# Performance work log

Measured on AMD Instinct MI355X. Metric: run time of the kernel, lower is better.

Reference implementation:

```python
import jax, jax.numpy as jnp
import numpy as np

BLANK_ID = 0


def bias_norm(x, bias, log_scale):
    # icefall BiasNorm: x * exp(log_scale) / rms(x - bias), rms over channel dim
    scales = jnp.exp(log_scale) * jax.lax.rsqrt(
        jnp.mean(jnp.square(x - bias), axis=-1, keepdims=True))
    return x * scales


def setup_inputs() -> dict:
    key = jax.random.key(0)
    N, T, S = 16, 400, 5
    ENC, DEC, JOINT, V = 512, 512, 512, 2000
    OV = V - 1  # out_vocab_dim
    ks = jax.random.split(key, 16)
    f = jax.random.normal
    return {
        "encoder_out": f(ks[0], (N, T, S, ENC), jnp.float32),
        "blank_decoder_out": f(ks[1], (N, T, S, DEC), jnp.float32),
        "vocab_decoder_out": f(ks[2], (N, T, S, DEC), jnp.float32),
        # fc_encoder_proj + its BiasNorm
        "W_enc": f(ks[3], (JOINT, ENC), jnp.float32) * 0.02,
        "b_enc": jnp.zeros((JOINT,), jnp.float32),
        "bn_enc_bias": f(ks[4], (JOINT,), jnp.float32) * 0.01,
        "bn_enc_log_scale": jnp.zeros((), jnp.float32),
        # fc_blank_decoder + its BiasNorm
        "W_bdec": f(ks[5], (JOINT, DEC), jnp.float32) * 0.02,
        "b_bdec": jnp.zeros((JOINT,), jnp.float32),
        "bn_bdec_bias": f(ks[6], (JOINT,), jnp.float32) * 0.01,
        "bn_bdec_log_scale": jnp.zeros((), jnp.float32),
        # BiasNorm for vocab decoder path (over decoder_hidden_dim)
        "bn_vdec_bias": f(ks[7], (DEC,), jnp.float32) * 0.01,
        "bn_vdec_log_scale": jnp.zeros((), jnp.float32),
        # output heads
        "W_blank": f(ks[8], (1, JOINT), jnp.float32) * 0.02,
        "b_blank": jnp.zeros((1,), jnp.float32),
        "W_ev": f(ks[9], (OV, JOINT), jnp.float32) * 0.02,
        "b_ev": jnp.zeros((OV,), jnp.float32),
        "W_dv": f(ks[10], (OV, JOINT), jnp.float32) * 0.02,
        "b_dv": jnp.zeros((OV,), jnp.float32),
    }


def reference(encoder_out, blank_decoder_out, vocab_decoder_out,
              W_enc, b_enc, bn_enc_bias, bn_enc_log_scale,
              W_bdec, b_bdec, bn_bdec_bias, bn_bdec_log_scale,
              bn_vdec_bias, bn_vdec_log_scale,
              W_blank, b_blank, W_ev, b_ev, W_dv, b_dv):
    # encoder_proj: ScaledLinear -> BiasNorm
    enc = bias_norm(jnp.einsum('ntsc,jc->ntsj', encoder_out, W_enc) + b_enc,
                    bn_enc_bias, bn_enc_log_scale)
    # blank_decoder_proj: ScaledLinear -> BiasNorm
    bdec = bias_norm(jnp.einsum('ntsc,jc->ntsj', blank_decoder_out, W_bdec) + b_bdec,
                     bn_bdec_bias, bn_bdec_log_scale)
    # vocab_decoder_proj: BiasNorm -> ScaledLinear -> log_softmax
    vdec = bias_norm(vocab_decoder_out, bn_vdec_bias, bn_vdec_log_scale)
    vdec = jnp.einsum('ntsj,vj->ntsv', vdec, W_dv) + b_dv
    vocab_decoder_prob = jax.nn.log_softmax(vdec, axis=-1)
    # joint
    blank_prob = jnp.einsum('ntsj,oj->ntso', jax.nn.relu(enc + bdec), W_blank) + b_blank
    vocab_prob = jnp.einsum('ntsj,vj->ntsv', enc, W_ev) + b_ev + vocab_decoder_prob
    out = jnp.concatenate(
        [vocab_prob[..., :BLANK_ID], blank_prob, vocab_prob[..., BLANK_ID:]], axis=-1)
    return out, vocab_decoder_prob
```

## Files before the change

kernel.cpp:

```cpp
#include <hip/hip_runtime.h>


#define R_TOTAL 32000
#define OV 1999
#define WG_ROWS 2049

typedef __attribute__((ext_vector_type(8))) short bh8;
typedef __attribute__((ext_vector_type(4))) float fx4;

__device__ __forceinline__ unsigned short f2bf(float f) {
  union { float f; unsigned u; } v; v.f = f;
  unsigned r = v.u + 0x7fffu + ((v.u >> 16) & 1u);
  return (unsigned short)(r >> 16);
}
__device__ __forceinline__ float bf2f(unsigned short h) {
  union { unsigned u; float f; } v; v.u = ((unsigned)h) << 16;
  return v.f;
}
__device__ __forceinline__ void gload_lds16(const void* g, void* l) {
  __builtin_amdgcn_global_load_lds(
      (__attribute__((address_space(1))) void*)g,
      (__attribute__((address_space(3))) void*)l, 16, 0, 0);
}
__device__ __forceinline__ void st16u(float* dst, const float* src) {
  float v[4] = {src[0], src[1], src[2], src[3]};
  __builtin_memcpy((void*)dst, v, 16);
}

__global__ void wconv_kernel(const float* __restrict__ src, unsigned short* __restrict__ dst,
                             int src_rows, int dst_rows, int shift) {
  long long n = (long long)dst_rows * 512;
  for (long long i = (long long)blockIdx.x * blockDim.x + threadIdx.x; i < n;
       i += (long long)gridDim.x * blockDim.x) {
    int row = (int)(i >> 9);
    int sr = row - shift;
    dst[i] = (sr >= 0 && sr < src_rows) ? f2bf(src[(long long)sr * 512 + (i & 511)])
                                        : (unsigned short)0;
  }
}

template<int MODE>
__global__ __launch_bounds__(1024)
void proj_norm_kernel(const float* __restrict__ X,
                      const unsigned short* __restrict__ Wb,
                      const float* __restrict__ b_lin,
                      const float* __restrict__ bn_bias,
                      const float* __restrict__ log_scale,
                      unsigned short* __restrict__ enc_b,
                      const float* __restrict__ W_blank,
                      const float* __restrict__ b_blank,
                      float* __restrict__ blank)
{
  __shared__ __attribute__((aligned(16))) unsigned short As[128 * 64];
  __shared__ __attribute__((aligned(16))) unsigned short Bs[512 * 64];
  __shared__ float red[8][128];
  __shared__ float scale_s[128];

  const int tid = threadIdx.x;
  const int l  = tid & 63;
  const int lq = l >> 4;
  const int lr = l & 15;
  const int w  = tid >> 6;
  const int wr = w >> 3;
  const int wc = w & 7;
  const int rowBase = blockIdx.x * 128;

  char* AsB = (char*)As;
  char* BsB = (char*)Bs;

  fx4 acc[4][4];
#pragma unroll
  for (int m = 0; m < 4; ++m)
#pragma unroll
    for (int n = 0; n < 4; ++n)
#pragma unroll
      for (int r = 0; r < 4; ++r) acc[m][n][r] = 0.f;

  for (int kt = 0; kt < 8; ++kt) {
#pragma unroll
    for (int p = 0; p < 2; ++p) {
      int g = tid + p * 1024;
      int row = g >> 4;
      int c4  = g & 15;
      const float4 v = *(const float4*)(X + (long long)(rowBase + row) * 512 + kt * 64 + c4 * 4);
      ushort4 h;
      h.x = f2bf(v.x); h.y = f2bf(v.y); h.z = f2bf(v.z); h.w = f2bf(v.w);
      *(ushort4*)(AsB + row * 128 + ((c4 * 8) ^ ((row & 7) << 4))) = h;
    }
#pragma unroll
    for (int p = 0; p < 4; ++p) {
      int gb = (w * 4 + p) * 64;
      int g = gb + l;
      int row = g >> 3;
      int c8 = (g & 7) ^ (row & 7);
      gload_lds16(Wb + (long long)row * 512 + kt * 64 + c8 * 8, BsB + gb * 16);
    }
    __syncthreads();

#pragma unroll
    for (int kk = 0; kk < 2; ++kk) {
      const int kb = (kk * 32 + lq * 8) * 2;
      bh8 a[4];
#pragma unroll
      for (int m = 0; m < 4; ++m) {
        int row = wr * 64 + m * 16 + lr;
        a[m] = *(const bh8*)(AsB + row * 128 + (kb ^ ((row & 7) << 4)));
      }
#pragma unroll
      for (int n = 0; n < 4; ++n) {
        int brow = wc * 64 + n * 16 + lr;
        bh8 bfr = *(const bh8*)(BsB + brow * 128 + (kb ^ ((brow & 7) << 4)));
#pragma unroll
        for (int m = 0; m < 4; ++m)
          acc[m][n] = __builtin_amdgcn_mfma_f32_16x16x32_bf16(a[m], bfr, acc[m][n], 0, 0, 0);
      }
    }
    __syncthreads();
  }

  const float escale = expf(log_scale[0]);
  float bl[4], bb[4], wb[4];
#pragma unroll
  for (int n = 0; n < 4; ++n) {
    int col = wc * 64 + n * 16 + lr;
    bl[n] = b_lin[col];
    bb[n] = bn_bias[col];
    if (MODE == 1) wb[n] = W_blank[col];
  }

  float ps[4][4];
#pragma unroll
  for (int m = 0; m < 4; ++m)
#pragma unroll
    for (int r = 0; r < 4; ++r) ps[m][r] = 0.f;
#pragma unroll
  for (int m = 0; m < 4; ++m)
#pragma unroll
    for (int n = 0; n < 4; ++n)
#pragma unroll
      for (int r = 0; r < 4; ++r) {
        float v = acc[m][n][r] + bl[n];
        float d = v - bb[n];
        ps[m][r] += d * d;
      }
#pragma unroll
  for (int off = 1; off < 16; off <<= 1)
#pragma unroll
    for (int m = 0; m < 4; ++m)
#pragma unroll
      for (int r = 0; r < 4; ++r)
        ps[m][r] += __shfl_xor(ps[m][r], off);

  if (lr == 0) {
#pragma unroll
    for (int m = 0; m < 4; ++m)
#pragma unroll
      for (int r = 0; r < 4; ++r)
        red[wc][wr * 64 + m * 16 + lq * 4 + r] = ps[m][r];
  }
  __syncthreads();
  if (tid < 128) {
    float s = 0.f;
#pragma unroll
    for (int c = 0; c < 8; ++c) s += red[c][tid];
    scale_s[tid] = escale * rsqrtf(s * (1.0f / 512.0f));
  }
  __syncthreads();

  if (MODE == 0) {
#pragma unroll
    for (int m = 0; m < 4; ++m)
#pragma unroll
      for (int n = 0; n < 4; ++n)
#pragma unroll
        for (int r = 0; r < 4; ++r) {
          int rl = wr * 64 + m * 16 + lq * 4 + r;
          int col = wc * 64 + n * 16 + lr;
          float v = (acc[m][n][r] + bl[n]) * scale_s[rl];
          enc_b[(long long)(rowBase + rl) * 512 + col] = f2bf(v);
        }
  } else {
    float pb[4][4];
#pragma unroll
    for (int m = 0; m < 4; ++m)
#pragma unroll
      for (int r = 0; r < 4; ++r) pb[m][r] = 0.f;
#pragma unroll
    for (int m = 0; m < 4; ++m)
#pragma unroll
      for (int n = 0; n < 4; ++n)
#pragma unroll
        for (int r = 0; r < 4; ++r) {
          int rl = wr * 64 + m * 16 + lq * 4 + r;
          int col = wc * 64 + n * 16 + lr;
          float v = (acc[m][n][r] + bl[n]) * scale_s[rl];
          float e = bf2f(enc_b[(long long)(rowBase + rl) * 512 + col]);
          float s = e + v;
          s = s > 0.f ? s : 0.f;
          pb[m][r] += s * wb[n];
        }
#pragma unroll
    for (int off = 1; off < 16; off <<= 1)
#pragma unroll
      for (int m = 0; m < 4; ++m)
#pragma unroll
        for (int r = 0; r < 4; ++r)
          pb[m][r] += __shfl_xor(pb[m][r], off);
    if (lr == 0) {
#pragma unroll
      for (int m = 0; m < 4; ++m)
#pragma unroll
        for (int r = 0; r < 4; ++r)
          red[wc][wr * 64 + m * 16 + lq * 4 + r] = pb[m][r];
    }
    __syncthreads();
    if (tid < 128) {
      float s = 0.f;
#pragma unroll
      for (int c = 0; c < 8; ++c) s += red[c][tid];
      blank[rowBase + tid] = s + b_blank[0];
    }
  }
}

__global__ __launch_bounds__(256)
void vdec_norm_kernel(const float* __restrict__ X, const float* __restrict__ bn_bias,
                      const float* __restrict__ log_scale, unsigned short* __restrict__ dst)
{
  const int l = threadIdx.x & 63;
  const long long row = (long long)blockIdx.x * 4 + (threadIdx.x >> 6);
  const float* xr = X + row * 512 + l * 8;
  float4 v0 = *(const float4*)xr;
  float4 v1 = *(const float4*)(xr + 4);
  float xv[8] = {v0.x, v0.y, v0.z, v0.w, v1.x, v1.y, v1.z, v1.w};
  const float4 b0 = *(const float4*)(bn_bias + l * 8);
  const float4 b1 = *(const float4*)(bn_bias + l * 8 + 4);
  float bv[8] = {b0.x, b0.y, b0.z, b0.w, b1.x, b1.y, b1.z, b1.w};
  float s = 0.f;
#pragma unroll
  for (int i = 0; i < 8; ++i) { float d = xv[i] - bv[i]; s += d * d; }
#pragma unroll
  for (int off = 1; off < 64; off <<= 1) s += __shfl_xor(s, off);
  const float sc = expf(log_scale[0]) * rsqrtf(s * (1.0f / 512.0f));
  bh8 o;
#pragma unroll
  for (int i = 0; i < 8; ++i) o[i] = (short)f2bf(xv[i] * sc);
  *(bh8*)(dst + row * 512 + l * 8) = o;
}

__device__ __forceinline__ void xcd_swz_250x16(int& bx, int& by) {
  int bid = blockIdx.y * 250 + blockIdx.x;
  int g = (bid & 7) * 500 + (bid >> 3);
  bx = g >> 4;
  by = g & 15;
}

__global__ __launch_bounds__(256, 2)
void gemm_stats_kernel(const unsigned short* __restrict__ Abf,
                       const unsigned short* __restrict__ Wb,
                       const float* __restrict__ bias,
                       float2* __restrict__ stats)
{
  __shared__ __attribute__((aligned(16))) unsigned short As[128 * 64];
  __shared__ __attribute__((aligned(16))) unsigned short Bs[128 * 64];
  __shared__ float smax[2][128];
  __shared__ float ssum[2][128];
  const int tid = threadIdx.x;
  const int l  = tid & 63, lq = l >> 4, lr = l & 15;
  const int w  = tid >> 6;
  const int wr = w >> 1, wc = w & 1;
  int bx, by;
  xcd_swz_250x16(bx, by);
  const int rowBase = bx * 128;
  const int colBase = by * 128;
  char* AsB = (char*)As;
  char* BsB = (char*)Bs;

  fx4 acc[4][4];
#pragma unroll
  for (int m = 0; m < 4; ++m)
#pragma unroll
    for (int n = 0; n < 4; ++n)
#pragma unroll
      for (int r = 0; r < 4; ++r) acc[m][n][r] = 0.f;

  for (int kt = 0; kt < 8; ++kt) {
#pragma unroll
    for (int p = 0; p < 4; ++p) {
      int gb = (w * 4 + p) * 64;
      int g = gb + l;
      int row = g >> 3;
      int c8 = (g & 7) ^ (row & 7);
      gload_lds16(Abf + (long long)(rowBase + row) * 512 + kt * 64 + c8 * 8, AsB + gb * 16);
      gload_lds16(Wb  + (long long)(colBase + row) * 512 + kt * 64 + c8 * 8, BsB + gb * 16);
    }
    __syncthreads();
#pragma unroll
    for (int kk = 0; kk < 2; ++kk) {
      const int kb = (kk * 32 + lq * 8) * 2;
      bh8 a[4];
#pragma unroll
      for (int m = 0; m < 4; ++m) {
        int row = wr * 64 + m * 16 + lr;
        a[m] = *(const bh8*)(AsB + row * 128 + (kb ^ ((row & 7) << 4)));
      }
#pragma unroll
      for (int n = 0; n < 4; ++n) {
        int brow = wc * 64 + n * 16 + lr;
        bh8 bfr = *(const bh8*)(BsB + brow * 128 + (kb ^ ((brow & 7) << 4)));
#pragma unroll
        for (int m = 0; m < 4; ++m)
          acc[m][n] = __builtin_amdgcn_mfma_f32_16x16x32_bf16(a[m], bfr, acc[m][n], 0, 0, 0);
      }
    }
    __syncthreads();
  }

  float bl[4]; bool cv[4];
#pragma unroll
  for (int n = 0; n < 4; ++n) {
    int col = colBase + wc * 64 + n * 16 + lr;
    cv[n] = (col < OV);
    bl[n] = cv[n] ? bias[col] : 0.f;
  }

  float mloc[4][4];
#pragma unroll
  for (int m = 0; m < 4; ++m)
#pragma unroll
    for (int r = 0; r < 4; ++r) mloc[m][r] = -3.4e38f;
#pragma unroll
  for (int m = 0; m < 4; ++m)
#pragma unroll
    for (int n = 0; n < 4; ++n)
      if (cv[n])
#pragma unroll
        for (int r = 0; r < 4; ++r)
          mloc[m][r] = fmaxf(mloc[m][r], acc[m][n][r] + bl[n]);
#pragma unroll
  for (int off = 1; off < 16; off <<= 1)
#pragma unroll
    for (int m = 0; m < 4; ++m)
#pragma unroll
      for (int r = 0; r < 4; ++r)
        mloc[m][r] = fmaxf(mloc[m][r], __shfl_xor(mloc[m][r], off));
  if (lr == 0) {
#pragma unroll
    for (int m = 0; m < 4; ++m)
#pragma unroll
      for (int r = 0; r < 4; ++r)
        smax[wc][wr * 64 + m * 16 + lq * 4 + r] = mloc[m][r];
  }
  __syncthreads();
  float M[4][4];
#pragma unroll
  for (int m = 0; m < 4; ++m)
#pragma unroll
    for (int r = 0; r < 4; ++r) {
      int row = wr * 64 + m * 16 + lq * 4 + r;
      M[m][r] = fmaxf(smax[0][row], smax[1][row]);
    }
  float sl[4][4];
#pragma unroll
  for (int m = 0; m < 4; ++m)
#pragma unroll
    for (int r = 0; r < 4; ++r) sl[m][r] = 0.f;
#pragma unroll
  for (int m = 0; m < 4; ++m)
#pragma unroll
    for (int n = 0; n < 4; ++n)
      if (cv[n]) {
#pragma unroll
        for (int r = 0; r < 4; ++r) {
          float v = acc[m][n][r] + bl[n];
          sl[m][r] += __expf(v - M[m][r]);
        }
      }
#pragma unroll
  for (int off = 1; off < 16; off <<= 1)
#pragma unroll
    for (int m = 0; m < 4; ++m)
#pragma unroll
      for (int r = 0; r < 4; ++r)
        sl[m][r] += __shfl_xor(sl[m][r], off);
  if (lr == 0) {
#pragma unroll
    for (int m = 0; m < 4; ++m)
#pragma unroll
      for (int r = 0; r < 4; ++r)
        ssum[wc][wr * 64 + m * 16 + lq * 4 + r] = sl[m][r];
  }
  __syncthreads();
  if (tid < 128) {
    float2 st;
    st.x = fmaxf(smax[0][tid], smax[1][tid]);
    st.y = ssum[0][tid] + ssum[1][tid];
    stats[(long long)by * R_TOTAL + rowBase + tid] = st;
  }
}

__global__ __launch_bounds__(256)
void lz_kernel(const float2* __restrict__ stats, float* __restrict__ lz)
{
  int row = blockIdx.x * 256 + threadIdx.x;
  if (row >= R_TOTAL) return;
  float2 st[16];
  float M = -3.4e38f;
#pragma unroll
  for (int i = 0; i < 16; ++i) {
    st[i] = stats[(long long)i * R_TOTAL + row];
    M = fmaxf(M, st[i].x);
  }
  float S = 0.f;
#pragma unroll
  for (int i = 0; i < 16; ++i) S += st[i].y * __expf(st[i].x - M);
  lz[row] = M + logf(S);
}

__global__ __launch_bounds__(256, 2)
void gemm_fused_kernel(const unsigned short* __restrict__ Av_g,
                       const unsigned short* __restrict__ Ae_g,
                       const unsigned short* __restrict__ Wdv_g,
                       const unsigned short* __restrict__ Wev_g,
                       const float* __restrict__ b_dv,
                       const float* __restrict__ b_ev,
                       const float* __restrict__ lz,
                       const float* __restrict__ blank,
                       float* __restrict__ vdp,
                       float* __restrict__ outp)
{
  __shared__ __attribute__((aligned(16))) unsigned short As[128 * 64];
  __shared__ __attribute__((aligned(16))) unsigned short Bs[128 * 64];
  const int tid = threadIdx.x;
  const int l  = tid & 63, lq = l >> 4, lr = l & 15;
  const int w  = tid >> 6;
  const int wr = w >> 1, wc = w & 1;
  int bx, by;
  xcd_swz_250x16(bx, by);
  const int rowBase = bx * 128;
  const int colBase = by * 128;
  char* AsB = (char*)As;
  char* BsB = (char*)Bs;

  fx4 accV[4][4], accE[4][4];
#pragma unroll
  for (int m = 0; m < 4; ++m)
#pragma unroll
    for (int n = 0; n < 4; ++n)
#pragma unroll
      for (int r = 0; r < 4; ++r) { accV[m][n][r] = 0.f; accE[m][n][r] = 0.f; }

  for (int kt = 0; kt < 8; ++kt) {
#pragma unroll
    for (int p = 0; p < 4; ++p) {
      int gb = (w * 4 + p) * 64;
      int g = gb + l;
      int row = g >> 3;
      int c8 = (g & 7) ^ (row & 7);
      gload_lds16(Av_g  + (long long)(rowBase + row) * 512 + kt * 64 + c8 * 8, AsB + gb * 16);
      gload_lds16(Wdv_g + (long long)(colBase + row) * 512 + kt * 64 + c8 * 8, BsB + gb * 16);
    }
    __syncthreads();
#pragma unroll
    for (int kk = 0; kk < 2; ++kk) {
      const int kb = (kk * 32 + lq * 8) * 2;
      bh8 a[4];
#pragma unroll
      for (int m = 0; m < 4; ++m) {
        int row = wr * 64 + m * 16 + lr;
        a[m] = *(const bh8*)(AsB + row * 128 + (kb ^ ((row & 7) << 4)));
      }
#pragma unroll
      for (int n = 0; n < 4; ++n) {
        int brow = wc * 64 + n * 16 + lr;
        bh8 bfr = *(const bh8*)(BsB + brow * 128 + (kb ^ ((brow & 7) << 4)));
#pragma unroll
        for (int m = 0; m < 4; ++m)
          accV[m][n] = __builtin_amdgcn_mfma_f32_16x16x32_bf16(a[m], bfr, accV[m][n], 0, 0, 0);
      }
    }
    __syncthreads();
  }

  for (int kt = 0; kt < 8; ++kt) {
#pragma unroll
    for (int p = 0; p < 4; ++p) {
      int gb = (w * 4 + p) * 64;
      int g = gb + l;
      int row = g >> 3;
      int c8 = (g & 7) ^ (row & 7);
      gload_lds16(Ae_g  + (long long)(rowBase + row) * 512 + kt * 64 + c8 * 8, AsB + gb * 16);
      gload_lds16(Wev_g + (long long)(colBase + row) * 512 + kt * 64 + c8 * 8, BsB + gb * 16);
    }
    __syncthreads();
#pragma unroll
    for (int kk = 0; kk < 2; ++kk) {
      const int kb = (kk * 32 + lq * 8) * 2;
      bh8 a[4];
#pragma unroll
      for (int m = 0; m < 4; ++m) {
        int row = wr * 64 + m * 16 + lr;
        a[m] = *(const bh8*)(AsB + row * 128 + (kb ^ ((row & 7) << 4)));
      }
#pragma unroll
      for (int n = 0; n < 4; ++n) {
        int brow = wc * 64 + n * 16 + lr;
        bh8 bfr = *(const bh8*)(BsB + brow * 128 + (kb ^ ((brow & 7) << 4)));
#pragma unroll
        for (int m = 0; m < 4; ++m)
          accE[m][n] = __builtin_amdgcn_mfma_f32_16x16x32_bf16(a[m], bfr, accE[m][n], 0, 0, 0);
      }
    }
    __syncthreads();
  }

  float lzv[4][4];
#pragma unroll
  for (int m = 0; m < 4; ++m)
#pragma unroll
    for (int r = 0; r < 4; ++r)
      lzv[m][r] = lz[rowBase + wr * 64 + m * 16 + lq * 4 + r];

  float* Lvd = (float*)As;
  float* Lov = (float*)Bs;

  const int c0 = (by == 0) ? 0 : (colBase - 1);
  const int j0 = (by == 0) ? 1 : 0;
  const int Lv = min(OV, colBase + 127) - c0;

  const int flipw = (lq & 1) << 4;

#pragma unroll
  for (int c = 0; c < 4; ++c) {
    __syncthreads();
    if (wr == (c >> 1)) {
#pragma unroll
      for (int mm = 0; mm < 2; ++mm) {
        const int m = (c & 1) * 2 + mm;
#pragma unroll
        for (int n = 0; n < 4; ++n) {
          int j = wc * 64 + n * 16 + lr;
          int cg = colBase - 1 + j;
          bool v = (cg >= 0 && cg < OV);
          float bdv = v ? b_dv[cg] : 0.f;
          float bev = v ? b_ev[cg] : 0.f;
          int jx = j ^ flipw;
#pragma unroll
          for (int r = 0; r < 4; ++r) {
            int lrow = 16 * mm + lq * 4 + r;
            float vd = accV[m][n][r] + bdv - lzv[m][r];
            float ov = accE[m][n][r] + bev + vd;
            if (by == 0 && j == 0) ov = blank[rowBase + 32 * c + lrow];
            Lvd[lrow * 128 + jx] = vd;
            Lov[lrow * 128 + jx] = ov;
          }
        }
      }
    }
    __syncthreads();

#pragma unroll
    for (int pass = 0; pass < 4; ++pass) {
      int lrow = pass * 8 + (tid >> 5);
      int lane32 = tid & 31;
      int flip = ((lrow >> 2) & 1) << 4;
      long long rg = rowBase + 32 * c + lrow;
      int p = colBase + lane32 * 4;
      if (p < 2000) {
        float4 vv = *(const float4*)&Lov[lrow * 128 + ((lane32 * 4) ^ flip)];
        *(float4*)(outp + rg * 2000 + p) = vv;
      }
    }
#pragma unroll
    for (int pass = 0; pass < 4; ++pass) {
      int lrow = pass * 8 + (tid >> 5);
      int lane32 = tid & 31;
      int flip = ((lrow >> 2) & 1) << 4;
      long long rg = rowBase + 32 * c + lrow;
      int k4 = lane32 * 4;
      if (k4 < Lv) {
        float* dst = vdp + rg * OV + c0 + k4;
        int rem = Lv - k4;
        if (rem >= 4 && j0 == 0) {
          float4 vv = *(const float4*)&Lvd[lrow * 128 + (k4 ^ flip)];
          float vs[4] = {vv.x, vv.y, vv.z, vv.w};
          st16u(dst, vs);
        } else if (rem >= 4) {
          float vs[4];
#pragma unroll
          for (int q = 0; q < 4; ++q) vs[q] = Lvd[lrow * 128 + ((j0 + k4 + q) ^ flip)];
          st16u(dst, vs);
        } else {
          for (int q = 0; q < rem; ++q) dst[q] = Lvd[lrow * 128 + ((j0 + k4 + q) ^ flip)];
        }
      }
    }
  }
}

extern "C" void kernel_launch(void* const* d_in, const int* in_sizes, int n_in,
                              void* d_out, int out_size, void* d_ws, size_t ws_size,
                              hipStream_t stream) {
  const float* encoder_out  = (const float*)d_in[0];
  const float* blank_dec    = (const float*)d_in[1];
  const float* vocab_dec    = (const float*)d_in[2];
  const float* W_enc        = (const float*)d_in[3];
  const float* b_enc        = (const float*)d_in[4];
  const float* bn_enc_bias  = (const float*)d_in[5];
  const float* bn_enc_ls    = (const float*)d_in[6];
  const float* W_bdec       = (const float*)d_in[7];
  const float* b_bdec       = (const float*)d_in[8];
  const float* bn_bdec_bias = (const float*)d_in[9];
  const float* bn_bdec_ls   = (const float*)d_in[10];
  const float* bn_vdec_bias = (const float*)d_in[11];
  const float* bn_vdec_ls   = (const float*)d_in[12];
  const float* W_blank      = (const float*)d_in[13];
  const float* b_blank      = (const float*)d_in[14];
  const float* W_ev         = (const float*)d_in[15];
  const float* b_ev         = (const float*)d_in[16];
  const float* W_dv         = (const float*)d_in[17];
  const float* b_dv         = (const float*)d_in[18];

  unsigned short* Wenc_b  = (unsigned short*)d_ws;
  unsigned short* Wbdec_b = Wenc_b + 512 * 512;
  unsigned short* Wdv_g   = Wbdec_b + 512 * 512;
  unsigned short* Wev_g   = Wdv_g + (size_t)WG_ROWS * 512;
  unsigned short* enc_b   = Wev_g + (size_t)WG_ROWS * 512;
  unsigned short* vdec_b  = enc_b + (size_t)R_TOTAL * 512;
  float2* stats = (float2*)(vdec_b + (size_t)R_TOTAL * 512);
  float*  lzbuf = (float*)(stats + (size_t)R_TOTAL * 16);
  float*  blank = lzbuf + R_TOTAL;

  float* outp = (float*)d_out;
  float* vdp  = outp + (size_t)R_TOTAL * 2000;

  wconv_kernel<<<256, 256, 0, stream>>>(W_enc,  Wenc_b,  512, 512, 0);
  wconv_kernel<<<256, 256, 0, stream>>>(W_bdec, Wbdec_b, 512, 512, 0);
  wconv_kernel<<<512, 256, 0, stream>>>(W_dv,   Wdv_g,  1999, WG_ROWS, 1);
  wconv_kernel<<<512, 256, 0, stream>>>(W_ev,   Wev_g,  1999, WG_ROWS, 1);

  vdec_norm_kernel<<<8000, 256, 0, stream>>>(vocab_dec, bn_vdec_bias, bn_vdec_ls, vdec_b);
  gemm_stats_kernel<<<dim3(250, 16), 256, 0, stream>>>(vdec_b, Wdv_g + 512, b_dv, stats);
  lz_kernel<<<125, 256, 0, stream>>>(stats, lzbuf);

  proj_norm_kernel<0><<<250, 1024, 0, stream>>>(encoder_out, Wenc_b, b_enc, bn_enc_bias,
                                                bn_enc_ls, enc_b, nullptr, nullptr, nullptr);
  proj_norm_kernel<1><<<250, 1024, 0, stream>>>(blank_dec, Wbdec_b, b_bdec, bn_bdec_bias,
                                                bn_bdec_ls, enc_b, W_blank, b_blank, blank);

  gemm_fused_kernel<<<dim3(250, 16), 256, 0, stream>>>(vdec_b, enc_b, Wdv_g, Wev_g,
                                                       b_dv, b_ev, lzbuf, blank, vdp, outp);
}
```

Measured before the change: 557.7 us.

## Restructure vocab GEMMs as row-persistent blocks looping over all column tiles

```diff
diff --git a/kernel.cpp b/kernel.cpp
--- a/kernel.cpp
+++ b/kernel.cpp
@@ -248,176 +248,144 @@
   *(bh8*)(dst + row * 512 + l * 8) = o;
 }
 
-__device__ __forceinline__ void xcd_swz_250x16(int& bx, int& by) {
-  int bid = blockIdx.y * 250 + blockIdx.x;
-  int g = (bid & 7) * 500 + (bid >> 3);
-  bx = g >> 4;
-  by = g & 15;
-}
-
-__global__ __launch_bounds__(256, 2)
-void gemm_stats_kernel(const unsigned short* __restrict__ Abf,
-                       const unsigned short* __restrict__ Wb,
-                       const float* __restrict__ bias,
-                       float2* __restrict__ stats)
+__global__ __launch_bounds__(512, 2)
+void stats_kernel(const unsigned short* __restrict__ Av_g,
+                  const unsigned short* __restrict__ Wb,
+                  const float* __restrict__ bias,
+                  float* __restrict__ lzout)
 {
-  __shared__ __attribute__((aligned(16))) unsigned short As[128 * 64];
-  __shared__ __attribute__((aligned(16))) unsigned short Bs[128 * 64];
-  __shared__ float smax[2][128];
-  __shared__ float ssum[2][128];
+  __shared__ __attribute__((aligned(16))) unsigned short Wbs[2][128 * 64];
   const int tid = threadIdx.x;
   const int l  = tid & 63, lq = l >> 4, lr = l & 15;
   const int w  = tid >> 6;
-  const int wr = w >> 1, wc = w & 1;
-  int bx, by;
-  xcd_swz_250x16(bx, by);
-  const int rowBase = bx * 128;
-  const int colBase = by * 128;
-  char* AsB = (char*)As;
-  char* BsB = (char*)Bs;
-
-  fx4 acc[4][4];
-#pragma unroll
-  for (int m = 0; m < 4; ++m)
-#pragma unroll
-    for (int n = 0; n < 4; ++n)
-#pragma unroll
-      for (int r = 0; r < 4; ++r) acc[m][n][r] = 0.f;
-
-  for (int kt = 0; kt < 8; ++kt) {
-#pragma unroll
-    for (int p = 0; p < 4; ++p) {
-      int gb = (w * 4 + p) * 64;
-      int g = gb + l;
-      int row = g >> 3;
-      int c8 = (g & 7) ^ (row & 7);
-      gload_lds16(Abf + (long long)(rowBase + row) * 512 + kt * 64 + c8 * 8, AsB + gb * 16);
-      gload_lds16(Wb  + (long long)(colBase + row) * 512 + kt * 64 + c8 * 8, BsB + gb * 16);
+  const int wr = w >> 2;
+  const int wc = w & 3;
+  const int rowBase = blockIdx.x * 64;
+
+  bh8 avf[2][8][2];
+#pragma unroll
+  for (int m = 0; m < 2; ++m) {
+    const unsigned short* rp = Av_g + (long long)(rowBase + wr * 32 + m * 16 + lr) * 512;
+#pragma unroll
+    for (int kt = 0; kt < 8; ++kt)
+#pragma unroll
+      for (int kk = 0; kk < 2; ++kk)
+        avf[m][kt][kk] = *(const bh8*)(rp + kt * 64 + kk * 32 + lq * 8);
+  }
+
+  float Mx[2][4], Sx[2][4];
+#pragma unroll
+  for (int m = 0; m < 2; ++m)
+#pragma unroll
+    for (int r = 0; r < 4; ++r) { Mx[m][r] = -3.4e38f; Sx[m][r] = 0.f; }
+
+  for (int by = 0; by < 16; ++by) {
+    fx4 acc[2][2];
+#pragma unroll
+    for (int m = 0; m < 2; ++m)
+#pragma unroll
+      for (int n = 0; n < 2; ++n)
+#pragma unroll
+        for (int r = 0; r < 4; ++r) acc[m][n][r] = 0.f;
+
+#pragma unroll
+    for (int p = 0; p < 2; ++p) {
+      int lc = p * 512 + tid;
+      int rW = lc >> 3, c = lc & 7;
+      int cs = c ^ (rW & 7);
+      gload_lds16(Wb + (long long)(by * 128 + rW) * 512 + 0 * 64 + cs * 8,
+                  (char*)Wbs[0] + lc * 16);
     }
     __syncthreads();
-#pragma unroll
-    for (int kk = 0; kk < 2; ++kk) {
-      const int kb = (kk * 32 + lq * 8) * 2;
-      bh8 a[4];
-#pragma unroll
-      for (int m = 0; m < 4; ++m) {
-        int row = wr * 64 + m * 16 + lr;
-        a[m] = *(const bh8*)(AsB + row * 128 + (kb ^ ((row & 7) << 4)));
-      }
-#pragma unroll
-      for (int n = 0; n < 4; ++n) {
-        int brow = wc * 64 + n * 16 + lr;
-        bh8 bfr = *(const bh8*)(BsB + brow * 128 + (kb ^ ((brow & 7) << 4)));
-#pragma unroll
-        for (int m = 0; m < 4; ++m)
-          acc[m][n] = __builtin_amdgcn_mfma_f32_16x16x32_bf16(a[m], bfr, acc[m][n], 0, 0, 0);
-      }
-    }
-    __syncthreads();
-  }
-
-  float bl[4]; bool cv[4];
-#pragma unroll
-  for (int n = 0; n < 4; ++n) {
-    int col = colBase + wc * 64 + n * 16 + lr;
-    cv[n] = (col < OV);
-    bl[n] = cv[n] ? bias[col] : 0.f;
-  }
-
-  float mloc[4][4];
-#pragma unroll
-  for (int m = 0; m < 4; ++m)
-#pragma unroll
-    for (int r = 0; r < 4; ++r) mloc[m][r] = -3.4e38f;
-#pragma unroll
-  for (int m = 0; m < 4; ++m)
-#pragma unroll
-    for (int n = 0; n < 4; ++n)
-      if (cv[n])
-#pragma unroll
-        for (int r = 0; r < 4; ++r)
-          mloc[m][r] = fmaxf(mloc[m][r], acc[m][n][r] + bl[n]);
+
+#pragma unroll
+    for (int kt = 0; kt < 8; ++kt) {
+      if (kt < 7) {
+#pragma unroll
+        for (int p = 0; p < 2; ++p) {
+          int lc = p * 512 + tid;
+          int rW = lc >> 3, c = lc & 7;
+          int cs = c ^ (rW & 7);
+          gload_lds16(Wb + (long long)(by * 128 + rW) * 512 + (kt + 1) * 64 + cs * 8,
+                      (char*)Wbs[(kt + 1) & 1] + lc * 16);
+        }
+      }
+      char* WB = (char*)Wbs[kt & 1];
+#pragma unroll
+      for (int kk = 0; kk < 2; ++kk) {
+#pragma unroll
+        for (int n = 0; n < 2; ++n) {
+          int br = wc * 32 + n * 16 + lr;
+          bh8 bf = *(const bh8*)(WB + br * 128 + (((kk * 4 + lq) ^ (br & 7)) * 16));
+          acc[0][n] = __builtin_amdgcn_mfma_f32_16x16x32_bf16(avf[0][kt][kk], bf, acc[0][n], 0, 0, 0);
+          acc[1][n] = __builtin_amdgcn_mfma_f32_16x16x32_bf16(avf[1][kt][kk], bf, acc[1][n], 0, 0, 0);
+        }
+      }
+      __syncthreads();
+    }
+
+    int col0 = by * 128 + wc * 32 + lr;
+    int col1 = col0 + 16;
+    bool cv0 = col0 < OV, cv1 = col1 < OV;
+    float bl0 = cv0 ? bias[col0] : 0.f;
+    float bl1 = cv1 ? bias[col1] : 0.f;
+#pragma unroll
+    for (int m = 0; m < 2; ++m)
+#pragma unroll
+      for (int r = 0; r < 4; ++r) {
+        float v0 = acc[m][0][r] + bl0;
+        float v1 = acc[m][1][r] + bl1;
+        float pm = -3.4e38f;
+        if (cv0) pm = v0;
+        if (cv1) pm = fmaxf(pm, v1);
+        float s = 0.f;
+        if (cv0) s += __expf(v0 - pm);
+        if (cv1) s += __expf(v1 - pm);
+        float Mn = fmaxf(Mx[m][r], pm);
+        Sx[m][r] = Sx[m][r] * __expf(Mx[m][r] - Mn) + s * __expf(pm - Mn);
+        Mx[m][r] = Mn;
+      }
+  }
+
 #pragma unroll
   for (int off = 1; off < 16; off <<= 1)
 #pragma unroll
-    for (int m = 0; m < 4; ++m)
-#pragma unroll
-      for (int r = 0; r < 4; ++r)
-        mloc[m][r] = fmaxf(mloc[m][r], __shfl_xor(mloc[m][r], off));
+    for (int m = 0; m < 2; ++m)
+#pragma unroll
+      for (int r = 0; r < 4; ++r) {
+        float Mo = __shfl_xor(Mx[m][r], off);
+        float So = __shfl_xor(Sx[m][r], off);
+        float Mn = fmaxf(Mx[m][r], Mo);
+        Sx[m][r] = Sx[m][r] * __expf(Mx[m][r] - Mn) + So * __expf(Mo - Mn);
+        Mx[m][r] = Mn;
+      }
+
+  float2* red = (float2*)Wbs;
+  __syncthreads();
   if (lr == 0) {
 #pragma unroll
-    for (int m = 0; m < 4; ++m)
-#pragma unroll
-      for (int r = 0; r < 4; ++r)
-        smax[wc][wr * 64 + m * 16 + lq * 4 + r] = mloc[m][r];
+    for (int m = 0; m < 2; ++m)
+#pragma unroll
+      for (int r = 0; r < 4; ++r) {
+        int row = wr * 32 + m * 16 + lq * 4 + r;
+        red[wc * 64 + row] = make_float2(Mx[m][r], Sx[m][r]);
+      }
   }
   __syncthreads();
-  float M[4][4];
-#pragma unroll
-  for (int m = 0; m < 4; ++m)
-#pragma unroll
-    for (int r = 0; r < 4; ++r) {
-      int row = wr * 64 + m * 16 + lq * 4 + r;
-      M[m][r] = fmaxf(smax[0][row], smax[1][row]);
-    }
-  float sl[4][4];
-#pragma unroll
-  for (int m = 0; m < 4; ++m)
-#pragma unroll
-    for (int r = 0; r < 4; ++r) sl[m][r] = 0.f;
-#pragma unroll
-  for (int m = 0; m < 4; ++m)
-#pragma unroll
-    for (int n = 0; n < 4; ++n)
-      if (cv[n]) {
-#pragma unroll
-        for (int r = 0; r < 4; ++r) {
-          float v = acc[m][n][r] + bl[n];
-          sl[m][r] += __expf(v - M[m][r]);
-        }
-      }
-#pragma unroll
-  for (int off = 1; off < 16; off <<= 1)
-#pragma unroll
-    for (int m = 0; m < 4; ++m)
-#pragma unroll
-      for (int r = 0; r < 4; ++r)
-        sl[m][r] += __shfl_xor(sl[m][r], off);
-  if (lr == 0) {
-#pragma unroll
-    for (int m = 0; m < 4; ++m)
-#pragma unroll
-      for (int r = 0; r < 4; ++r)
-        ssum[wc][wr * 64 + m * 16 + lq * 4 + r] = sl[m][r];
-  }
-  __syncthreads();
-  if (tid < 128) {
-    float2 st;
-    st.x = fmaxf(smax[0][tid], smax[1][tid]);
-    st.y = ssum[0][tid] + ssum[1][tid];
-    stats[(long long)by * R_TOTAL + rowBase + tid] = st;
-  }
-}
-
-__global__ __launch_bounds__(256)
-void lz_kernel(const float2* __restrict__ stats, float* __restrict__ lz)
-{
-  int row = blockIdx.x * 256 + threadIdx.x;
-  if (row >= R_TOTAL) return;
-  float2 st[16];
-  float M = -3.4e38f;
-#pragma unroll
-  for (int i = 0; i < 16; ++i) {
-    st[i] = stats[(long long)i * R_TOTAL + row];
-    M = fmaxf(M, st[i].x);
-  }
-  float S = 0.f;
-#pragma unroll
-  for (int i = 0; i < 16; ++i) S += st[i].y * __expf(st[i].x - M);
-  lz[row] = M + logf(S);
-}
-
-__global__ __launch_bounds__(256, 2)
+  if (tid < 64) {
+    float M = -3.4e38f, S = 0.f;
+#pragma unroll
+    for (int c = 0; c < 4; ++c) {
+      float2 st = red[c * 64 + tid];
+      float Mn = fmaxf(M, st.x);
+      S = S * __expf(M - Mn) + st.y * __expf(st.x - Mn);
+      M = Mn;
+    }
+    lzout[rowBase + tid] = M + logf(S);
+  }
+}
+
+__global__ __launch_bounds__(512, 2)
 void gemm_fused_kernel(const unsigned short* __restrict__ Av_g,
                        const unsigned short* __restrict__ Ae_g,
                        const unsigned short* __restrict__ Wdv_g,
@@ -429,171 +397,192 @@
                        float* __restrict__ vdp,
                        float* __restrict__ outp)
 {
-  __shared__ __attribute__((aligned(16))) unsigned short As[128 * 64];
-  __shared__ __attribute__((aligned(16))) unsigned short Bs[128 * 64];
+  __shared__ __attribute__((aligned(16))) unsigned short Aes[64 * 512];
+  __shared__ __attribute__((aligned(16))) unsigned short Wbs[2][128 * 64];
   const int tid = threadIdx.x;
   const int l  = tid & 63, lq = l >> 4, lr = l & 15;
   const int w  = tid >> 6;
-  const int wr = w >> 1, wc = w & 1;
-  int bx, by;
-  xcd_swz_250x16(bx, by);
-  const int rowBase = bx * 128;
-  const int colBase = by * 128;
-  char* AsB = (char*)As;
-  char* BsB = (char*)Bs;
-
-  fx4 accV[4][4], accE[4][4];
-#pragma unroll
-  for (int m = 0; m < 4; ++m)
-#pragma unroll
-    for (int n = 0; n < 4; ++n)
-#pragma unroll
-      for (int r = 0; r < 4; ++r) { accV[m][n][r] = 0.f; accE[m][n][r] = 0.f; }
-
-  for (int kt = 0; kt < 8; ++kt) {
-#pragma unroll
-    for (int p = 0; p < 4; ++p) {
-      int gb = (w * 4 + p) * 64;
-      int g = gb + l;
-      int row = g >> 3;
-      int c8 = (g & 7) ^ (row & 7);
-      gload_lds16(Av_g  + (long long)(rowBase + row) * 512 + kt * 64 + c8 * 8, AsB + gb * 16);
-      gload_lds16(Wdv_g + (long long)(colBase + row) * 512 + kt * 64 + c8 * 8, BsB + gb * 16);
+  const int wr = w >> 2;
+  const int wc = w & 3;
+  const int rowBase = blockIdx.x * 64;
+  char* AeB = (char*)Aes;
+
+  bh8 avf[2][8][2];
+#pragma unroll
+  for (int m = 0; m < 2; ++m) {
+    const unsigned short* rp = Av_g + (long long)(rowBase + wr * 32 + m * 16 + lr) * 512;
+#pragma unroll
+    for (int kt = 0; kt < 8; ++kt)
+#pragma unroll
+      for (int kk = 0; kk < 2; ++kk)
+        avf[m][kt][kk] = *(const bh8*)(rp + kt * 64 + kk * 32 + lq * 8);
+  }
+
+#pragma unroll
+  for (int p = 0; p < 8; ++p) {
+    int lc = p * 512 + tid;
+    int r = lc >> 6, c = lc & 63;
+    int csrc = (c & 56) | ((c & 7) ^ (r & 7));
+    gload_lds16(Ae_g + (long long)(rowBase + r) * 512 + csrc * 8, AeB + lc * 16);
+  }
+
+  float lzv[2][4];
+#pragma unroll
+  for (int m = 0; m < 2; ++m)
+#pragma unroll
+    for (int r = 0; r < 4; ++r)
+      lzv[m][r] = lz[rowBase + wr * 32 + m * 16 + lq * 4 + r];
+
+  __syncthreads();
+
+  for (int by = 0; by < 16; ++by) {
+    fx4 accV[2][2], accE[2][2];
+#pragma unroll
+    for (int m = 0; m < 2; ++m)
+#pragma unroll
+      for (int n = 0; n < 2; ++n)
+#pragma unroll
+        for (int r = 0; r < 4; ++r) { accV[m][n][r] = 0.f; accE[m][n][r] = 0.f; }
+
+#pragma unroll
+    for (int p = 0; p < 2; ++p) {
+      int lc = p * 512 + tid;
+      int rW = lc >> 3, c = lc & 7;
+      int cs = c ^ (rW & 7);
+      gload_lds16(Wdv_g + (long long)(by * 128 + rW) * 512 + cs * 8,
+                  (char*)Wbs[0] + lc * 16);
     }
     __syncthreads();
 #pragma unroll
-    for (int kk = 0; kk < 2; ++kk) {
-      const int kb = (kk * 32 + lq * 8) * 2;
-      bh8 a[4];
-#pragma unroll
-      for (int m = 0; m < 4; ++m) {
-        int row = wr * 64 + m * 16 + lr;
-        a[m] = *(const bh8*)(AsB + row * 128 + (kb ^ ((row & 7) << 4)));
-      }
-#pragma unroll
-      for (int n = 0; n < 4; ++n) {
-        int brow = wc * 64 + n * 16 + lr;
-        bh8 bfr = *(const bh8*)(BsB + brow * 128 + (kb ^ ((brow & 7) << 4)));
-#pragma unroll
-        for (int m = 0; m < 4; ++m)
-          accV[m][n] = __builtin_amdgcn_mfma_f32_16x16x32_bf16(a[m], bfr, accV[m][n], 0, 0, 0);
-      }
+    for (int kt = 0; kt < 8; ++kt) {
+      if (kt < 7) {
+#pragma unroll
+        for (int p = 0; p < 2; ++p) {
+          int lc = p * 512 + tid;
+          int rW = lc >> 3, c = lc & 7;
+          int cs = c ^ (rW & 7);
+          gload_lds16(Wdv_g + (long long)(by * 128 + rW) * 512 + (kt + 1) * 64 + cs * 8,
+                      (char*)Wbs[(kt + 1) & 1] + lc * 16);
+        }
+      }
+      char* WB = (char*)Wbs[kt & 1];
+#pragma unroll
+      for (int kk = 0; kk < 2; ++kk) {
+#pragma unroll
+        for (int n = 0; n < 2; ++n) {
+          int br = wc * 32 + n * 16 + lr;
+          bh8 bf = *(const bh8*)(WB + br * 128 + (((kk * 4 + lq) ^ (br & 7)) * 16));
+          accV[0][n] = __builtin_amdgcn_mfma_f32_16x16x32_bf16(avf[0][kt][kk], bf, accV[0][n], 0, 0, 0);
+          accV[1][n] = __builtin_amdgcn_mfma_f32_16x16x32_bf16(avf[1][kt][kk], bf, accV[1][n], 0, 0, 0);
+        }
+      }
+      __syncthreads();
+    }
+
+#pragma unroll
+    for (int p = 0; p < 2; ++p) {
+      int lc = p * 512 + tid;
+      int rW = lc >> 3, c = lc & 7;
+      int cs = c ^ (rW & 7);
+      gload_lds16(Wev_g + (long long)(by * 128 + rW) * 512 + cs * 8,
+                  (char*)Wbs[0] + lc * 16);
     }
     __syncthreads();
-  }
-
-  for (int kt = 0; kt < 8; ++kt) {
-#pragma unroll
-    for (int p = 0; p < 4; ++p) {
-      int gb = (w * 4 + p) * 64;
-      int g = gb + l;
-      int row = g >> 3;
-      int c8 = (g & 7) ^ (row & 7);
-      gload_lds16(Ae_g  + (long long)(rowBase + row) * 512 + kt * 64 + c8 * 8, AsB + gb * 16);
-      gload_lds16(Wev_g + (long long)(colBase + row) * 512 + kt * 64 + c8 * 8, BsB + gb * 16);
-    }
-    __syncthreads();
-#pragma unroll
-    for (int kk = 0; kk < 2; ++kk) {
-      const int kb = (kk * 32 + lq * 8) * 2;
-      bh8 a[4];
-#pragma unroll
-      for (int m = 0; m < 4; ++m) {
-        int row = wr * 64 + m * 16 + lr;
-        a[m] = *(const bh8*)(AsB + row * 128 + (kb ^ ((row & 7) << 4)));
-      }
-#pragma unroll
-      for (int n = 0; n < 4; ++n) {
-        int brow = wc * 64 + n * 16 + lr;
-        bh8 bfr = *(const bh8*)(BsB + brow * 128 + (kb ^ ((brow & 7) << 4)));
-#pragma unroll
-        for (int m = 0; m < 4; ++m)
-          accE[m][n] = __builtin_amdgcn_mfma_f32_16x16x32_bf16(a[m], bfr, accE[m][n], 0, 0, 0);
-      }
-    }
-    __syncthreads();
-  }
-
-  float lzv[4][4];
-#pragma unroll
-  for (int m = 0; m < 4; ++m)
-#pragma unroll
-    for (int r = 0; r < 4; ++r)
-      lzv[m][r] = lz[rowBase + wr * 64 + m * 16 + lq * 4 + r];
-
-  float* Lvd = (float*)As;
-  float* Lov = (float*)Bs;
-
-  const int c0 = (by == 0) ? 0 : (colBase - 1);
-  const int j0 = (by == 0) ? 1 : 0;
-  const int Lv = min(OV, colBase + 127) - c0;
-
-  const int flipw = (lq & 1) << 4;
-
-#pragma unroll
-  for (int c = 0; c < 4; ++c) {
-    __syncthreads();
-    if (wr == (c >> 1)) {
-#pragma unroll
-      for (int mm = 0; mm < 2; ++mm) {
-        const int m = (c & 1) * 2 + mm;
-#pragma unroll
-        for (int n = 0; n < 4; ++n) {
-          int j = wc * 64 + n * 16 + lr;
-          int cg = colBase - 1 + j;
-          bool v = (cg >= 0 && cg < OV);
-          float bdv = v ? b_dv[cg] : 0.f;
-          float bev = v ? b_ev[cg] : 0.f;
-          int jx = j ^ flipw;
-#pragma unroll
-          for (int r = 0; r < 4; ++r) {
-            int lrow = 16 * mm + lq * 4 + r;
-            float vd = accV[m][n][r] + bdv - lzv[m][r];
-            float ov = accE[m][n][r] + bev + vd;
-            if (by == 0 && j == 0) ov = blank[rowBase + 32 * c + lrow];
-            Lvd[lrow * 128 + jx] = vd;
-            Lov[lrow * 128 + jx] = ov;
+#pragma unroll
+    for (int kt = 0; kt < 8; ++kt) {
+      if (kt < 7) {
+#pragma unroll
+        for (int p = 0; p < 2; ++p) {
+          int lc = p * 512 + tid;
+          int rW = lc >> 3, c = lc & 7;
+          int cs = c ^ (rW & 7);
+          gload_lds16(Wev_g + (long long)(by * 128 + rW) * 512 + (kt + 1) * 64 + cs * 8,
+                      (char*)Wbs[(kt + 1) & 1] + lc * 16);
+        }
+      }
+      char* WB = (char*)Wbs[kt & 1];
+#pragma unroll
+      for (int kk = 0; kk < 2; ++kk) {
+        bh8 ae[2];
+#pragma unroll
+        for (int m = 0; m < 2; ++m) {
+          int ar = wr * 32 + m * 16 + lr;
+          int ph = kt * 8 + ((kk * 4 + lq) ^ (ar & 7));
+          ae[m] = *(const bh8*)(AeB + ar * 1024 + ph * 16);
+        }
+#pragma unroll
+        for (int n = 0; n < 2; ++n) {
+          int br = wc * 32 + n * 16 + lr;
+          bh8 bf = *(const bh8*)(WB + br * 128 + (((kk * 4 + lq) ^ (br & 7)) * 16));
+          accE[0][n] = __builtin_amdgcn_mfma_f32_16x16x32_bf16(ae[0], bf, accE[0][n], 0, 0, 0);
+          accE[1][n] = __builtin_amdgcn_mfma_f32_16x16x32_bf16(ae[1], bf, accE[1][n], 0, 0, 0);
+        }
+      }
+      __syncthreads();
+    }
+
+    float* Lvd = (float*)Wbs;
+    float* Lov = Lvd + 32 * 128;
+    const int colBase = by * 128;
+    const int c0 = (by == 0) ? 0 : (colBase - 1);
+    const int j0 = (by == 0) ? 1 : 0;
+    const int Lv = min(OV, colBase + 127) - c0;
+
+#pragma unroll
+    for (int c = 0; c < 2; ++c) {
+      if (wr == c) {
+#pragma unroll
+        for (int m = 0; m < 2; ++m)
+#pragma unroll
+          for (int n = 0; n < 2; ++n) {
+            int j = wc * 32 + n * 16 + lr;
+            int cg = colBase - 1 + j;
+            bool v = (cg >= 0 && cg < OV);
+            float bdv = v ? b_dv[cg] : 0.f;
+            float bev = v ? b_ev[cg] : 0.f;
+            int jx = j ^ ((lq & 1) << 4);
+#pragma unroll
+            for (int r = 0; r < 4; ++r) {
+              int lrow = m * 16 + lq * 4 + r;
+              float vd = accV[m][n][r] + bdv - lzv[m][r];
+              float ov = accE[m][n][r] + bev + vd;
+              if (by == 0 && j == 0) ov = blank[rowBase + c * 32 + lrow];
+              Lvd[lrow * 128 + jx] = vd;
+              Lov[lrow * 128 + jx] = ov;
+            }
           }
-        }
-      }
-    }
-    __syncthreads();
-
-#pragma unroll
-    for (int pass = 0; pass < 4; ++pass) {
-      int lrow = pass * 8 + (tid >> 5);
-      int lane32 = tid & 31;
-      int flip = ((lrow >> 2) & 1) << 4;
-      long long rg = rowBase + 32 * c + lrow;
-      int p = colBase + lane32 * 4;
-      if (p < 2000) {
-        float4 vv = *(const float4*)&Lov[lrow * 128 + ((lane32 * 4) ^ flip)];
-        *(float4*)(outp + rg * 2000 + p) = vv;
-      }
-    }
-#pragma unroll
-    for (int pass = 0; pass < 4; ++pass) {
-      int lrow = pass * 8 + (tid >> 5);
-      int lane32 = tid & 31;
-      int flip = ((lrow >> 2) & 1) << 4;
-      long long rg = rowBase + 32 * c + lrow;
-      int k4 = lane32 * 4;
-      if (k4 < Lv) {
-        float* dst = vdp + rg * OV + c0 + k4;
-        int rem = Lv - k4;
-        if (rem >= 4 && j0 == 0) {
-          float4 vv = *(const float4*)&Lvd[lrow * 128 + (k4 ^ flip)];
-          float vs[4] = {vv.x, vv.y, vv.z, vv.w};
-          st16u(dst, vs);
-        } else if (rem >= 4) {
-          float vs[4];
-#pragma unroll
-          for (int q = 0; q < 4; ++q) vs[q] = Lvd[lrow * 128 + ((j0 + k4 + q) ^ flip)];
-          st16u(dst, vs);
-        } else {
-          for (int q = 0; q < rem; ++q) dst[q] = Lvd[lrow * 128 + ((j0 + k4 + q) ^ flip)];
-        }
-      }
+      }
+      __syncthreads();
+#pragma unroll
+      for (int pass = 0; pass < 2; ++pass) {
+        int lrow = pass * 16 + (tid >> 5);
+        int lane32 = tid & 31;
+        int flip = ((lrow >> 2) & 1) << 4;
+        long long rg = rowBase + c * 32 + lrow;
+        int pcol = colBase + lane32 * 4;
+        if (pcol < 2000) {
+          float4 vv = *(const float4*)&Lov[lrow * 128 + ((lane32 * 4) ^ flip)];
+          *(float4*)(outp + rg * 2000 + pcol) = vv;
+        }
+        int k4 = lane32 * 4;
+        if (k4 < Lv) {
+          float* dst = vdp + rg * OV + c0 + k4;
+          int rem = Lv - k4;
+          if (rem >= 4 && j0 == 0) {
+            float4 vv = *(const float4*)&Lvd[lrow * 128 + (k4 ^ flip)];
+            float vs[4] = {vv.x, vv.y, vv.z, vv.w};
+            st16u(dst, vs);
+          } else if (rem >= 4) {
+            float vs[4];
+#pragma unroll
+            for (int q = 0; q < 4; ++q) vs[q] = Lvd[lrow * 128 + ((j0 + k4 + q) ^ flip)];
+            st16u(dst, vs);
+          } else {
+            for (int q = 0; q < rem; ++q) dst[q] = Lvd[lrow * 128 + ((j0 + k4 + q) ^ flip)];
+          }
+        }
+      }
+      __syncthreads();
     }
   }
 }
@@ -627,8 +616,7 @@
   unsigned short* Wev_g   = Wdv_g + (size_t)WG_ROWS * 512;
   unsigned short* enc_b   = Wev_g + (size_t)WG_ROWS * 512;
   unsigned short* vdec_b  = enc_b + (size_t)R_TOTAL * 512;
-  float2* stats = (float2*)(vdec_b + (size_t)R_TOTAL * 512);
-  float*  lzbuf = (float*)(stats + (size_t)R_TOTAL * 16);
+  float*  lzbuf = (float*)(vdec_b + (size_t)R_TOTAL * 512);
   float*  blank = lzbuf + R_TOTAL;
 
   float* outp = (float*)d_out;
@@ -640,14 +628,13 @@
   wconv_kernel<<<512, 256, 0, stream>>>(W_ev,   Wev_g,  1999, WG_ROWS, 1);
 
   vdec_norm_kernel<<<8000, 256, 0, stream>>>(vocab_dec, bn_vdec_bias, bn_vdec_ls, vdec_b);
-  gemm_stats_kernel<<<dim3(250, 16), 256, 0, stream>>>(vdec_b, Wdv_g + 512, b_dv, stats);
-  lz_kernel<<<125, 256, 0, stream>>>(stats, lzbuf);
+  stats_kernel<<<500, 512, 0, stream>>>(vdec_b, Wdv_g + 512, b_dv, lzbuf);
 
   proj_norm_kernel<0><<<250, 1024, 0, stream>>>(encoder_out, Wenc_b, b_enc, bn_enc_bias,
                                                 bn_enc_ls, enc_b, nullptr, nullptr, nullptr);
   proj_norm_kernel<1><<<250, 1024, 0, stream>>>(blank_dec, Wbdec_b, b_bdec, bn_bdec_bias,
                                                 bn_bdec_ls, enc_b, W_blank, b_blank, blank);
 
-  gemm_fused_kernel<<<dim3(250, 16), 256, 0, stream>>>(vdec_b, enc_b, Wdv_g, Wev_g,
-                                                       b_dv, b_ev, lzbuf, blank, vdp, outp);
-}
+  gemm_fused_kernel<<<500, 512, 0, stream>>>(vdec_b, enc_b, Wdv_g, Wev_g,
+                                             b_dv, b_ev, lzbuf, blank, vdp, outp);
+}
```

New measurement: 829.8 us. 48.8% more time.
